# Optimization experiments

Measured on AMD Instinct MI355X. Metric: run time of the kernel, lower is better.

Reference implementation:

```python
import jax, jax.numpy as jnp
import numpy as np

T, B, I, H = 128, 256, 512, 1024  # time, batch, input_size, hidden_size


def setup_inputs() -> dict:
    key = jax.random.key(0)
    k1, k2, k3, k4, k5 = jax.random.split(key, 5)
    s = 1.0 / np.sqrt(H)  # matches torch GRUCell uniform(-1/sqrt(H), 1/sqrt(H)) scale
    return {
        "input_seq": jax.random.normal(k1, (T, B, I), dtype=jnp.float32),
        "W_ih": jax.random.uniform(k2, (3 * H, I), minval=-s, maxval=s, dtype=jnp.float32),
        "W_hh": jax.random.uniform(k3, (3 * H, H), minval=-s, maxval=s, dtype=jnp.float32),
        "b_ih": jax.random.uniform(k4, (3 * H,), minval=-s, maxval=s, dtype=jnp.float32),
        "b_hh": jax.random.uniform(k5, (3 * H,), minval=-s, maxval=s, dtype=jnp.float32),
    }


def reference(input_seq, W_ih, W_hh, b_ih, b_hh):
    # Original torch code calls GRUCell(input_seq[i]) with NO hidden state and never
    # feeds the output back, so hx = 0 at EVERY step -> no recurrence; fully vectorizable.
    Hd = W_hh.shape[1]
    # input gates for all timesteps at once: (T, B, 3H)
    gi = jnp.einsum('tbi,gi->tbg', input_seq, W_ih) + b_ih
    # hidden gates with hx = 0: zeros @ W_hh.T + b_hh == b_hh broadcast, shape (B, 3H)
    h0 = jnp.zeros((input_seq.shape[1], Hd), dtype=input_seq.dtype)
    gh = h0 @ W_hh.T + b_hh
    i_r, i_z, i_n = gi[..., :Hd], gi[..., Hd:2 * Hd], gi[..., 2 * Hd:]
    h_r, h_z, h_n = gh[..., :Hd], gh[..., Hd:2 * Hd], gh[..., 2 * Hd:]
    r = jax.nn.sigmoid(i_r + h_r)
    z = jax.nn.sigmoid(i_z + h_z)
    n = jnp.tanh(i_n + r * h_n)
    h = (1.0 - z) * n + z * h0  # z*h0 == 0, kept for faithfulness
    # torch.stack(output, dim=1) -> (B, T, H)
    return jnp.transpose(h, (1, 0, 2))
```

## Files before the change

kernel.cpp:

```cpp
#include <hip/hip_runtime.h>
#include <hip/hip_bf16.h>

using f32x4  = __attribute__((ext_vector_type(4))) float;
using bf16x8 = __attribute__((ext_vector_type(8))) short;
using s16x4  = __attribute__((ext_vector_type(4))) short;

#define TT 128
#define BB 256
#define II 512
#define HH 1024
#define MM (TT * BB)

__device__ __forceinline__ short f2bf(float f) {
    unsigned u = __float_as_uint(f);
    u = u + 0x7FFFu + ((u >> 16) & 1u);
    return (short)(u >> 16);
}

__device__ __forceinline__ float sigmoid_f(float x) {
    float e = __expf(-fabsf(x));
    float s = 1.0f / (1.0f + e);
    return x >= 0.0f ? s : 1.0f - s;
}

__device__ __forceinline__ float tanh_f(float x) {
    float e = __expf(-2.0f * fabsf(x));
    float t = (1.0f - e) / (1.0f + e);
    return x >= 0.0f ? t : -t;
}

__device__ __forceinline__ void gload_lds16(const void* g, void* l) {
    __builtin_amdgcn_global_load_lds((const __attribute__((address_space(1))) unsigned*)g,
                                     (__attribute__((address_space(3))) unsigned*)l,
                                     16, 0, 0);
}

__global__ __launch_bounds__(256)
void cvt_both_kernel(const float* __restrict__ A, const float* __restrict__ W,
                     short* __restrict__ dst, int nA8, int nTot8) {
    const int stride = gridDim.x * blockDim.x;
    for (int i = blockIdx.x * blockDim.x + threadIdx.x; i < nTot8; i += stride) {
        const float* src = (i < nA8) ? (A + (size_t)i * 8) : (W + (size_t)(i - nA8) * 8);
        f32x4 v0 = ((const f32x4*)src)[0];
        f32x4 v1 = ((const f32x4*)src)[1];
        bf16x8 o;
        o[0] = f2bf(v0.x); o[1] = f2bf(v0.y); o[2] = f2bf(v0.z); o[3] = f2bf(v0.w);
        o[4] = f2bf(v1.x); o[5] = f2bf(v1.y); o[6] = f2bf(v1.z); o[7] = f2bf(v1.w);
        ((bf16x8*)dst)[i] = o;
    }
}

__global__ __launch_bounds__(512, 2)
void gru_gemm8_kernel(const short* __restrict__ Abf,
                      const short* __restrict__ Wbf,
                      const float* __restrict__ bih,
                      const float* __restrict__ bhh,
                      float* __restrict__ out)
{
    __shared__ char lds[114688];

    const int tid  = threadIdx.x;
    const int wid  = tid >> 6;
    const int lane = tid & 63;
    const int l15  = lane & 15;
    const int l4   = lane >> 4;
    const int wm   = wid >> 1;
    const int wn   = wid & 1;

    const int mtile = blockIdx.x >> 4;
    const int htile = blockIdx.x & 15;
    const int m0 = mtile * 256;
    const int h0 = htile * 64;

    const int lr8 = lane >> 3;
    const int lc  = lane & 7;
    const int csw = (lc * 16) ^ (lr8 << 4);

    const char* Ab = (const char*)Abf;
    const char* Wb = (const char*)Wbf;

    size_t aAddr[4];
    size_t wAddr[3];
    #pragma unroll
    for (int j = 0; j < 4; ++j)
        aAddr[j] = (size_t)(m0 + (wid * 4 + j) * 8 + lr8) * 1024 + csw;
    #pragma unroll
    for (int j = 0; j < 3; ++j) {
        const int row = (wid * 3 + j) * 8 + lr8;
        const int g   = row >> 6;
        const int wr  = row & 63;
        wAddr[j] = (size_t)(g * HH + h0 + wr) * 1024 + csw;
    }

    f32x4 acc[4][3][2];
    #pragma unroll
    for (int mf = 0; mf < 4; ++mf)
        #pragma unroll
        for (int g = 0; g < 3; ++g)
            #pragma unroll
            for (int nf = 0; nf < 2; ++nf)
                acc[mf][g][nf] = (f32x4){0.f, 0.f, 0.f, 0.f};

    #define STAGE(t, p)                                                          \
        do {                                                                     \
            const int kb_ = (t) * 128;                                           \
            _Pragma("unroll")                                                    \
            for (int j = 0; j < 4; ++j)                                          \
                gload_lds16(Ab + aAddr[j] + kb_,                                 \
                            lds + (p) * 32768 + (wid * 4 + j) * 1024);           \
            _Pragma("unroll")                                                    \
            for (int j = 0; j < 3; ++j)                                          \
                gload_lds16(Wb + wAddr[j] + kb_,                                 \
                            lds + 65536 + (p) * 24576 + (wid * 3 + j) * 1024);   \
        } while (0)

    STAGE(0, 0);

    const int xsw = (l15 & 7) << 4;

    for (int t = 0; t < 8; ++t) {
        const int p = t & 1;
        if (t < 7) {
            STAGE(t + 1, p ^ 1);
            asm volatile("s_waitcnt vmcnt(7)" ::: "memory");
        } else {
            asm volatile("s_waitcnt vmcnt(0)" ::: "memory");
        }
        __builtin_amdgcn_s_barrier();

        const char* Abase = lds + p * 32768;
        const char* Wbase = lds + 65536 + p * 24576;

        #pragma unroll
        for (int kk = 0; kk < 2; ++kk) {
            const int cb = kk * 64 + l4 * 16;
            bf16x8 a[4], b[3][2];
            #pragma unroll
            for (int mf = 0; mf < 4; ++mf) {
                const int r = wm * 64 + mf * 16 + l15;
                a[mf] = *(const bf16x8*)(Abase + r * 128 + (cb ^ xsw));
            }
            #pragma unroll
            for (int g = 0; g < 3; ++g)
                #pragma unroll
                for (int nf = 0; nf < 2; ++nf) {
                    const int rn = g * 64 + wn * 32 + nf * 16 + l15;
                    b[g][nf] = *(const bf16x8*)(Wbase + rn * 128 + (cb ^ xsw));
                }
            __builtin_amdgcn_s_setprio(1);
            #pragma unroll
            for (int mf = 0; mf < 4; ++mf)
                #pragma unroll
                for (int g = 0; g < 3; ++g)
                    #pragma unroll
                    for (int nf = 0; nf < 2; ++nf)
                        acc[mf][g][nf] = __builtin_amdgcn_mfma_f32_16x16x32_bf16(
                            a[mf], b[g][nf], acc[mf][g][nf], 0, 0, 0);
            __builtin_amdgcn_s_setprio(0);
        }
        asm volatile("" ::: "memory");
        __builtin_amdgcn_s_barrier();
    }
    #undef STAGE

    #pragma unroll
    for (int nf = 0; nf < 2; ++nf) {
        const int h = h0 + wn * 32 + nf * 16 + l15;
        const float bir = bih[h]          + bhh[h];
        const float biz = bih[HH + h]     + bhh[HH + h];
        const float bin = bih[2 * HH + h];
        const float bhn = bhh[2 * HH + h];
        #pragma unroll
        for (int mf = 0; mf < 4; ++mf) {
            const f32x4 ra = acc[mf][0][nf];
            const f32x4 za = acc[mf][1][nf];
            const f32x4 na = acc[mf][2][nf];
            #pragma unroll
            for (int j = 0; j < 4; ++j) {
                const int m = m0 + wm * 64 + mf * 16 + l4 * 4 + j;
                const int tt = m >> 8;
                const int bb = m & 255;
                const float r = sigmoid_f(ra[j] + bir);
                const float z = sigmoid_f(za[j] + biz);
                const float n = tanh_f(na[j] + bin + r * bhn);
                out[(size_t)bb * (TT * HH) + (size_t)tt * HH + h] = (1.0f - z) * n;
            }
        }
    }
}

__global__ __launch_bounds__(256, 2)
void gru_fused_kernel(const float* __restrict__ A,
                      const float* __restrict__ Wih,
                      const float* __restrict__ bih,
                      const float* __restrict__ bhh,
                      float* __restrict__ out)
{
    __shared__ short As[128 * 64];
    __shared__ short Ws[192 * 64];

    const int tid  = threadIdx.x;
    const int wid  = tid >> 6;
    const int lane = tid & 63;
    const int l15  = lane & 15;
    const int l4   = lane >> 4;

    const int mtile = blockIdx.x >> 4;
    const int htile = blockIdx.x & 15;
    const int m0 = mtile * 128;
    const int h0 = htile * 64;

    const int rbase = tid >> 4;
    const int c4    = tid & 15;
    const int swz   = (rbase & 7) << 3;

    f32x4 acc[2][12];
    #pragma unroll
    for (int i = 0; i < 2; ++i)
        #pragma unroll
        for (int j = 0; j < 12; ++j)
            acc[i][j] = (f32x4){0.f, 0.f, 0.f, 0.f};

    for (int kt = 0; kt < II / 64; ++kt) {
        const int k0 = kt * 64;
        __syncthreads();
        const float* Ab = A + (size_t)(m0 + rbase) * II + k0 + c4 * 4;
        #pragma unroll
        for (int i = 0; i < 8; ++i) {
            f32x4 v = *(const f32x4*)(Ab + (size_t)i * 16 * II);
            s16x4 hv;
            hv.x = f2bf(v.x); hv.y = f2bf(v.y); hv.z = f2bf(v.z); hv.w = f2bf(v.w);
            *(s16x4*)(As + (i * 16 + rbase) * 64 + ((c4 * 4) ^ swz)) = hv;
        }
        #pragma unroll
        for (int i = 0; i < 12; ++i) {
            const int row = i * 16 + rbase;
            const int g   = row >> 6;
            const int r   = row & 63;
            f32x4 v = *(const f32x4*)(Wih + (size_t)(g * HH + h0 + r) * II + k0 + c4 * 4);
            s16x4 hv;
            hv.x = f2bf(v.x); hv.y = f2bf(v.y); hv.z = f2bf(v.z); hv.w = f2bf(v.w);
            *(s16x4*)(Ws + row * 64 + ((c4 * 4) ^ swz)) = hv;
        }
        __syncthreads();

        #pragma unroll
        for (int kk = 0; kk < 2; ++kk) {
            const int kc = kk * 32 + l4 * 8;
            const int r0 = wid * 32 + l15;
            bf16x8 a0 = *(const bf16x8*)(As + r0 * 64 + (kc ^ ((r0 & 7) << 3)));
            bf16x8 a1 = *(const bf16x8*)(As + (r0 + 16) * 64 + (kc ^ ((r0 & 7) << 3)));
            #pragma unroll
            for (int nf = 0; nf < 12; ++nf) {
                const int rn = nf * 16 + l15;
                bf16x8 b = *(const bf16x8*)(Ws + rn * 64 + (kc ^ ((rn & 7) << 3)));
                acc[0][nf] = __builtin_amdgcn_mfma_f32_16x16x32_bf16(a0, b, acc[0][nf], 0, 0, 0);
                acc[1][nf] = __builtin_amdgcn_mfma_f32_16x16x32_bf16(a1, b, acc[1][nf], 0, 0, 0);
            }
        }
    }

    #pragma unroll
    for (int nf = 0; nf < 4; ++nf) {
        const int h = h0 + nf * 16 + l15;
        const float bir = bih[h]          + bhh[h];
        const float biz = bih[HH + h]     + bhh[HH + h];
        const float bin = bih[2 * HH + h];
        const float bhn = bhh[2 * HH + h];
        #pragma unroll
        for (int mf = 0; mf < 2; ++mf) {
            const f32x4 ra = acc[mf][nf];
            const f32x4 za = acc[mf][nf + 4];
            const f32x4 na = acc[mf][nf + 8];
            #pragma unroll
            for (int j = 0; j < 4; ++j) {
                const int m = m0 + wid * 32 + mf * 16 + l4 * 4 + j;
                const int tt = m >> 8;
                const int bb = m & 255;
                const float r = sigmoid_f(ra[j] + bir);
                const float z = sigmoid_f(za[j] + biz);
                const float n = tanh_f(na[j] + bin + r * bhn);
                out[(size_t)bb * (TT * HH) + (size_t)tt * HH + h] = (1.0f - z) * n;
            }
        }
    }
}

extern "C" void kernel_launch(void* const* d_in, const int* in_sizes, int n_in,
                              void* d_out, int out_size, void* d_ws, size_t ws_size,
                              hipStream_t stream) {
    const float* input = (const float*)d_in[0];
    const float* Wih   = (const float*)d_in[1];
    const float* bih   = (const float*)d_in[3];
    const float* bhh   = (const float*)d_in[4];
    float* out = (float*)d_out;

    const size_t nA = (size_t)MM * II;
    const size_t nW = (size_t)3 * HH * II;
    const size_t need = (nA + nW) * sizeof(short);

    if (ws_size >= need) {
        short* Abf = (short*)d_ws;
        cvt_both_kernel<<<4096, 256, 0, stream>>>(input, Wih, Abf,
                                                  (int)(nA / 8), (int)((nA + nW) / 8));
        const int nblocks = (MM / 256) * (HH / 64);
        gru_gemm8_kernel<<<nblocks, 512, 0, stream>>>(Abf, Abf + nA, bih, bhh, out);
    } else {
        const int nblocks = (MM / 128) * (HH / 64);
        gru_fused_kernel<<<nblocks, 256, 0, stream>>>(input, Wih, bih, bhh, out);
    }
}
```

Before: 341.2 us.

## Interleave global-to-LDS loads with MFMA phases and triple-buffer weights

Splits each K-tile of the GEMM into four MFMA phases and issues the next tile's A loads and the tile-after-next's W loads between them, with a triple-buffered W region in LDS (LDS grows to 136 KB). This is meant to hide global load latency behind matrix math rather than staging a whole tile up front. It also flips the block-index mapping so consecutive blocks share the same weight tile and walk different M tiles, which changes L2 reuse. The cost is more barriers per tile, and the larger LDS footprint may limit how many blocks fit on each CU.

```diff
diff --git a/kernel.cpp b/kernel.cpp
--- a/kernel.cpp
+++ b/kernel.cpp
@@ -51,13 +51,13 @@
 }
 
 __global__ __launch_bounds__(512, 2)
-void gru_gemm8_kernel(const short* __restrict__ Abf,
-                      const short* __restrict__ Wbf,
-                      const float* __restrict__ bih,
-                      const float* __restrict__ bhh,
-                      float* __restrict__ out)
+void gru_gemm8p_kernel(const short* __restrict__ Abf,
+                       const short* __restrict__ Wbf,
+                       const float* __restrict__ bih,
+                       const float* __restrict__ bhh,
+                       float* __restrict__ out)
 {
-    __shared__ char lds[114688];
+    __shared__ char lds[139264];
 
     const int tid  = threadIdx.x;
     const int wid  = tid >> 6;
@@ -67,8 +67,8 @@
     const int wm   = wid >> 1;
     const int wn   = wid & 1;
 
-    const int mtile = blockIdx.x >> 4;
-    const int htile = blockIdx.x & 15;
+    const int mtile = blockIdx.x & 127;
+    const int htile = blockIdx.x >> 7;
     const int m0 = mtile * 256;
     const int h0 = htile * 64;
 
@@ -92,6 +92,13 @@
         wAddr[j] = (size_t)(g * HH + h0 + wr) * 1024 + csw;
     }
 
+#define ABUF(p) ((char*)lds + (p) * 32768)
+#define WBUF(q) ((char*)lds + 65536 + (q) * 24576)
+#define GLA(u1, j) gload_lds16(Ab + aAddr[j] + (size_t)(u1) * 128, \
+                               ABUF((u1) & 1) + (wid * 4 + (j)) * 1024)
+#define GLW(u2, j) gload_lds16(Wb + wAddr[j] + (size_t)(u2) * 128, \
+                               WBUF((u2) % 3) + (wid * 3 + (j)) * 1024)
+
     f32x4 acc[4][3][2];
     #pragma unroll
     for (int mf = 0; mf < 4; ++mf)
@@ -101,67 +108,78 @@
             for (int nf = 0; nf < 2; ++nf)
                 acc[mf][g][nf] = (f32x4){0.f, 0.f, 0.f, 0.f};
 
-    #define STAGE(t, p)                                                          \
-        do {                                                                     \
-            const int kb_ = (t) * 128;                                           \
-            _Pragma("unroll")                                                    \
-            for (int j = 0; j < 4; ++j)                                          \
-                gload_lds16(Ab + aAddr[j] + kb_,                                 \
-                            lds + (p) * 32768 + (wid * 4 + j) * 1024);           \
-            _Pragma("unroll")                                                    \
-            for (int j = 0; j < 3; ++j)                                          \
-                gload_lds16(Wb + wAddr[j] + kb_,                                 \
-                            lds + 65536 + (p) * 24576 + (wid * 3 + j) * 1024);   \
-        } while (0)
-
-    STAGE(0, 0);
+    #pragma unroll
+    for (int j = 0; j < 3; ++j) GLW(0, j);
+    #pragma unroll
+    for (int j = 0; j < 4; ++j) GLA(0, j);
+    #pragma unroll
+    for (int j = 0; j < 3; ++j) GLW(1, j);
+    asm volatile("s_waitcnt vmcnt(3)" ::: "memory");
+    __builtin_amdgcn_s_barrier();
 
     const int xsw = (l15 & 7) << 4;
 
-    for (int t = 0; t < 8; ++t) {
-        const int p = t & 1;
-        if (t < 7) {
-            STAGE(t + 1, p ^ 1);
-            asm volatile("s_waitcnt vmcnt(7)" ::: "memory");
-        } else {
-            asm volatile("s_waitcnt vmcnt(0)" ::: "memory");
-        }
+#define PHASE_TAIL(NH)                                                        \
+    __builtin_amdgcn_s_barrier();                                             \
+    asm volatile("s_waitcnt lgkmcnt(0)" ::: "memory");                        \
+    __builtin_amdgcn_sched_barrier(0);                                        \
+    __builtin_amdgcn_s_setprio(1);                                            \
+    _Pragma("unroll")                                                         \
+    for (int mf = 0; mf < 4; ++mf)                                            \
+        _Pragma("unroll")                                                     \
+        for (int g = 0; g < 3; ++g)                                           \
+            acc[mf][g][NH] = __builtin_amdgcn_mfma_f32_16x16x32_bf16(         \
+                a[mf], b[g], acc[mf][g][NH], 0, 0, 0);                        \
+    __builtin_amdgcn_s_setprio(0);
+
+    #pragma unroll
+    for (int u = 0; u < 8; ++u) {
+        const char* Al = ABUF(u & 1);
+        const char* Wl = WBUF(u % 3);
+        bf16x8 a[4], b[3];
+
+        #pragma unroll
+        for (int mf = 0; mf < 4; ++mf)
+            a[mf] = *(const bf16x8*)(Al + (wm * 64 + mf * 16 + l15) * 128 + ((l4 * 16) ^ xsw));
+        #pragma unroll
+        for (int g = 0; g < 3; ++g)
+            b[g] = *(const bf16x8*)(Wl + (g * 64 + wn * 32 + l15) * 128 + ((l4 * 16) ^ xsw));
+        if (u < 7) { GLA(u + 1, 0); GLA(u + 1, 1); }
+        PHASE_TAIL(0)
         __builtin_amdgcn_s_barrier();
 
-        const char* Abase = lds + p * 32768;
-        const char* Wbase = lds + 65536 + p * 24576;
-
-        #pragma unroll
-        for (int kk = 0; kk < 2; ++kk) {
-            const int cb = kk * 64 + l4 * 16;
-            bf16x8 a[4], b[3][2];
-            #pragma unroll
-            for (int mf = 0; mf < 4; ++mf) {
-                const int r = wm * 64 + mf * 16 + l15;
-                a[mf] = *(const bf16x8*)(Abase + r * 128 + (cb ^ xsw));
-            }
-            #pragma unroll
-            for (int g = 0; g < 3; ++g)
-                #pragma unroll
-                for (int nf = 0; nf < 2; ++nf) {
-                    const int rn = g * 64 + wn * 32 + nf * 16 + l15;
-                    b[g][nf] = *(const bf16x8*)(Wbase + rn * 128 + (cb ^ xsw));
-                }
-            __builtin_amdgcn_s_setprio(1);
-            #pragma unroll
-            for (int mf = 0; mf < 4; ++mf)
-                #pragma unroll
-                for (int g = 0; g < 3; ++g)
-                    #pragma unroll
-                    for (int nf = 0; nf < 2; ++nf)
-                        acc[mf][g][nf] = __builtin_amdgcn_mfma_f32_16x16x32_bf16(
-                            a[mf], b[g][nf], acc[mf][g][nf], 0, 0, 0);
-            __builtin_amdgcn_s_setprio(0);
-        }
-        asm volatile("" ::: "memory");
+        #pragma unroll
+        for (int g = 0; g < 3; ++g)
+            b[g] = *(const bf16x8*)(Wl + (g * 64 + wn * 32 + 16 + l15) * 128 + ((l4 * 16) ^ xsw));
+        if (u < 7) { GLA(u + 1, 2); GLA(u + 1, 3); }
+        if (u < 6) { GLW(u + 2, 0); }
+        PHASE_TAIL(1)
         __builtin_amdgcn_s_barrier();
-    }
-    #undef STAGE
+
+        #pragma unroll
+        for (int mf = 0; mf < 4; ++mf)
+            a[mf] = *(const bf16x8*)(Al + (wm * 64 + mf * 16 + l15) * 128 + ((64 + l4 * 16) ^ xsw));
+        #pragma unroll
+        for (int g = 0; g < 3; ++g)
+            b[g] = *(const bf16x8*)(Wl + (g * 64 + wn * 32 + l15) * 128 + ((64 + l4 * 16) ^ xsw));
+        if (u < 6) { GLW(u + 2, 1); }
+        PHASE_TAIL(0)
+        __builtin_amdgcn_s_barrier();
+
+        #pragma unroll
+        for (int g = 0; g < 3; ++g)
+            b[g] = *(const bf16x8*)(Wl + (g * 64 + wn * 32 + 16 + l15) * 128 + ((64 + l4 * 16) ^ xsw));
+        if (u < 6) { GLW(u + 2, 2); }
+        PHASE_TAIL(1)
+        if (u < 6)      asm volatile("s_waitcnt vmcnt(3)" ::: "memory");
+        else if (u == 6) asm volatile("s_waitcnt vmcnt(0)" ::: "memory");
+        __builtin_amdgcn_s_barrier();
+    }
+#undef PHASE_TAIL
+#undef GLA
+#undef GLW
+#undef ABUF
+#undef WBUF
 
     #pragma unroll
     for (int nf = 0; nf < 2; ++nf) {
@@ -224,10 +242,10 @@
     for (int kt = 0; kt < II / 64; ++kt) {
         const int k0 = kt * 64;
         __syncthreads();
-        const float* Ab = A + (size_t)(m0 + rbase) * II + k0 + c4 * 4;
+        const float* Abp = A + (size_t)(m0 + rbase) * II + k0 + c4 * 4;
         #pragma unroll
         for (int i = 0; i < 8; ++i) {
-            f32x4 v = *(const f32x4*)(Ab + (size_t)i * 16 * II);
+            f32x4 v = *(const f32x4*)(Abp + (size_t)i * 16 * II);
             s16x4 hv;
             hv.x = f2bf(v.x); hv.y = f2bf(v.y); hv.z = f2bf(v.z); hv.w = f2bf(v.w);
             *(s16x4*)(As + (i * 16 + rbase) * 64 + ((c4 * 4) ^ swz)) = hv;
@@ -304,7 +322,7 @@
         cvt_both_kernel<<<4096, 256, 0, stream>>>(input, Wih, Abf,
                                                   (int)(nA / 8), (int)((nA + nW) / 8));
         const int nblocks = (MM / 256) * (HH / 64);
-        gru_gemm8_kernel<<<nblocks, 512, 0, stream>>>(Abf, Abf + nA, bih, bhh, out);
+        gru_gemm8p_kernel<<<nblocks, 512, 0, stream>>>(Abf, Abf + nA, bih, bhh, out);
     } else {
         const int nblocks = (MM / 128) * (HH / 64);
         gru_fused_kernel<<<nblocks, 256, 0, stream>>>(input, Wih, bih, bhh, out);
```

Measured after the change: 344.5 us. About the same (+1.0%).

## Shrink GEMM block tile to 128x192 with 4 waves and interleaved LDS loads

Applied to the files above, without the earlier changes.

Replaces the 8-wave 256-row block with a 4-wave, 128-row block in which each wave covers 32 rows against all 192 gate columns. LDS drops from 112 KB to 80 KB, and the grid becomes M-fastest so that blocks sharing a weight tile run together. The inner loop now interleaves each B-fragment LDS read with two MFMAs, and sched_barrier fences are added. The goal is better occupancy and latency hiding, at the cost of less A-tile reuse per block, since W is now loaded twice as often in total.

```diff
diff --git a/kernel.cpp b/kernel.cpp
--- a/kernel.cpp
+++ b/kernel.cpp
@@ -50,26 +50,24 @@
     }
 }
 
-__global__ __launch_bounds__(512, 2)
-void gru_gemm8_kernel(const short* __restrict__ Abf,
-                      const short* __restrict__ Wbf,
-                      const float* __restrict__ bih,
-                      const float* __restrict__ bhh,
-                      float* __restrict__ out)
+__global__ __launch_bounds__(256, 2)
+void gru_gemm_db_kernel(const short* __restrict__ Abf,
+                        const short* __restrict__ Wbf,
+                        const float* __restrict__ bih,
+                        const float* __restrict__ bhh,
+                        float* __restrict__ out)
 {
-    __shared__ char lds[114688];
+    __shared__ char lds[81920];
 
     const int tid  = threadIdx.x;
     const int wid  = tid >> 6;
     const int lane = tid & 63;
     const int l15  = lane & 15;
     const int l4   = lane >> 4;
-    const int wm   = wid >> 1;
-    const int wn   = wid & 1;
-
-    const int mtile = blockIdx.x >> 4;
-    const int htile = blockIdx.x & 15;
-    const int m0 = mtile * 256;
+
+    const int mtile = blockIdx.x & 255;
+    const int htile = blockIdx.x >> 8;
+    const int m0 = mtile * 128;
     const int h0 = htile * 64;
 
     const int lr8 = lane >> 3;
@@ -80,104 +78,91 @@
     const char* Wb = (const char*)Wbf;
 
     size_t aAddr[4];
-    size_t wAddr[3];
+    size_t wAddr[6];
     #pragma unroll
     for (int j = 0; j < 4; ++j)
         aAddr[j] = (size_t)(m0 + (wid * 4 + j) * 8 + lr8) * 1024 + csw;
     #pragma unroll
-    for (int j = 0; j < 3; ++j) {
-        const int row = (wid * 3 + j) * 8 + lr8;
+    for (int j = 0; j < 6; ++j) {
+        const int row = (wid * 6 + j) * 8 + lr8;
         const int g   = row >> 6;
         const int wr  = row & 63;
         wAddr[j] = (size_t)(g * HH + h0 + wr) * 1024 + csw;
     }
 
-    f32x4 acc[4][3][2];
-    #pragma unroll
-    for (int mf = 0; mf < 4; ++mf)
-        #pragma unroll
-        for (int g = 0; g < 3; ++g)
-            #pragma unroll
-            for (int nf = 0; nf < 2; ++nf)
-                acc[mf][g][nf] = (f32x4){0.f, 0.f, 0.f, 0.f};
-
-    #define STAGE(t, p)                                                          \
-        do {                                                                     \
-            const int kb_ = (t) * 128;                                           \
-            _Pragma("unroll")                                                    \
-            for (int j = 0; j < 4; ++j)                                          \
-                gload_lds16(Ab + aAddr[j] + kb_,                                 \
-                            lds + (p) * 32768 + (wid * 4 + j) * 1024);           \
-            _Pragma("unroll")                                                    \
-            for (int j = 0; j < 3; ++j)                                          \
-                gload_lds16(Wb + wAddr[j] + kb_,                                 \
-                            lds + 65536 + (p) * 24576 + (wid * 3 + j) * 1024);   \
-        } while (0)
+#define STAGE(t, p)                                                           \
+    do {                                                                      \
+        const int kb_ = (t) * 128;                                            \
+        _Pragma("unroll")                                                     \
+        for (int j = 0; j < 4; ++j)                                           \
+            gload_lds16(Ab + aAddr[j] + kb_,                                  \
+                        lds + (p) * 16384 + (wid * 4 + j) * 1024);            \
+        _Pragma("unroll")                                                     \
+        for (int j = 0; j < 6; ++j)                                           \
+            gload_lds16(Wb + wAddr[j] + kb_,                                  \
+                        lds + 32768 + (p) * 24576 + (wid * 6 + j) * 1024);    \
+    } while (0)
+
+    f32x4 acc[2][12];
+    #pragma unroll
+    for (int i = 0; i < 2; ++i)
+        #pragma unroll
+        for (int j = 0; j < 12; ++j)
+            acc[i][j] = (f32x4){0.f, 0.f, 0.f, 0.f};
 
     STAGE(0, 0);
 
     const int xsw = (l15 & 7) << 4;
 
+    #pragma unroll
     for (int t = 0; t < 8; ++t) {
         const int p = t & 1;
         if (t < 7) {
             STAGE(t + 1, p ^ 1);
-            asm volatile("s_waitcnt vmcnt(7)" ::: "memory");
+            asm volatile("s_waitcnt vmcnt(10)" ::: "memory");
         } else {
             asm volatile("s_waitcnt vmcnt(0)" ::: "memory");
         }
         __builtin_amdgcn_s_barrier();
-
-        const char* Abase = lds + p * 32768;
-        const char* Wbase = lds + 65536 + p * 24576;
+        __builtin_amdgcn_sched_barrier(0);
+
+        const char* Al = lds + p * 16384;
+        const char* Wl = lds + 32768 + p * 24576;
 
         #pragma unroll
         for (int kk = 0; kk < 2; ++kk) {
             const int cb = kk * 64 + l4 * 16;
-            bf16x8 a[4], b[3][2];
-            #pragma unroll
-            for (int mf = 0; mf < 4; ++mf) {
-                const int r = wm * 64 + mf * 16 + l15;
-                a[mf] = *(const bf16x8*)(Abase + r * 128 + (cb ^ xsw));
-            }
-            #pragma unroll
-            for (int g = 0; g < 3; ++g)
-                #pragma unroll
-                for (int nf = 0; nf < 2; ++nf) {
-                    const int rn = g * 64 + wn * 32 + nf * 16 + l15;
-                    b[g][nf] = *(const bf16x8*)(Wbase + rn * 128 + (cb ^ xsw));
-                }
-            __builtin_amdgcn_s_setprio(1);
-            #pragma unroll
-            for (int mf = 0; mf < 4; ++mf)
-                #pragma unroll
-                for (int g = 0; g < 3; ++g)
-                    #pragma unroll
-                    for (int nf = 0; nf < 2; ++nf)
-                        acc[mf][g][nf] = __builtin_amdgcn_mfma_f32_16x16x32_bf16(
-                            a[mf], b[g][nf], acc[mf][g][nf], 0, 0, 0);
-            __builtin_amdgcn_s_setprio(0);
-        }
-        asm volatile("" ::: "memory");
+            const int r0 = wid * 32 + l15;
+            bf16x8 a0 = *(const bf16x8*)(Al + r0 * 128 + (cb ^ xsw));
+            bf16x8 a1 = *(const bf16x8*)(Al + (r0 + 16) * 128 + (cb ^ xsw));
+            #pragma unroll
+            for (int nf = 0; nf < 12; ++nf) {
+                const int rn = nf * 16 + l15;
+                bf16x8 b = *(const bf16x8*)(Wl + rn * 128 + (cb ^ xsw));
+                acc[0][nf] = __builtin_amdgcn_mfma_f32_16x16x32_bf16(a0, b, acc[0][nf], 0, 0, 0);
+                acc[1][nf] = __builtin_amdgcn_mfma_f32_16x16x32_bf16(a1, b, acc[1][nf], 0, 0, 0);
+            }
+        }
+        __builtin_amdgcn_sched_barrier(0);
         __builtin_amdgcn_s_barrier();
     }
-    #undef STAGE
-
-    #pragma unroll
-    for (int nf = 0; nf < 2; ++nf) {
-        const int h = h0 + wn * 32 + nf * 16 + l15;
+#undef STAGE
+
+    #pragma unroll
+    for (int nf = 0; nf < 4; ++nf) {
+        const int h = h0 + nf * 16 + l15;
         const float bir = bih[h]          + bhh[h];
         const float biz = bih[HH + h]     + bhh[HH + h];
         const float bin = bih[2 * HH + h];
         const float bhn = bhh[2 * HH + h];
         #pragma unroll
-        for (int mf = 0; mf < 4; ++mf) {
-            const f32x4 ra = acc[mf][0][nf];
-            const f32x4 za = acc[mf][1][nf];
-            const f32x4 na = acc[mf][2][nf];
+        for (int mf = 0; mf < 2; ++mf) {
+            const f32x4 ra = acc[mf][nf];
+            const f32x4 za = acc[mf][nf + 4];
+            const f32x4 na = acc[mf][nf + 8];
             #pragma unroll
             for (int j = 0; j < 4; ++j) {
-                const int m = m0 + wm * 64 + mf * 16 + l4 * 4 + j;
+                const int m = m0 + wid * 32 + mf * 16 + l4 * 4 + j;
                 const int tt = m >> 8;
                 const int bb = m & 255;
                 const float r = sigmoid_f(ra[j] + bir);
@@ -224,10 +209,10 @@
     for (int kt = 0; kt < II / 64; ++kt) {
         const int k0 = kt * 64;
         __syncthreads();
-        const float* Ab = A + (size_t)(m0 + rbase) * II + k0 + c4 * 4;
+        const float* Abp = A + (size_t)(m0 + rbase) * II + k0 + c4 * 4;
         #pragma unroll
         for (int i = 0; i < 8; ++i) {
-            f32x4 v = *(const f32x4*)(Ab + (size_t)i * 16 * II);
+            f32x4 v = *(const f32x4*)(Abp + (size_t)i * 16 * II);
             s16x4 hv;
             hv.x = f2bf(v.x); hv.y = f2bf(v.y); hv.z = f2bf(v.z); hv.w = f2bf(v.w);
             *(s16x4*)(As + (i * 16 + rbase) * 64 + ((c4 * 4) ^ swz)) = hv;
@@ -303,8 +288,8 @@
         short* Abf = (short*)d_ws;
         cvt_both_kernel<<<4096, 256, 0, stream>>>(input, Wih, Abf,
                                                   (int)(nA / 8), (int)((nA + nW) / 8));
-        const int nblocks = (MM / 256) * (HH / 64);
-        gru_gemm8_kernel<<<nblocks, 512, 0, stream>>>(Abf, Abf + nA, bih, bhh, out);
+        const int nblocks = (MM / 128) * (HH / 64);
+        gru_gemm_db_kernel<<<nblocks, 256, 0, stream>>>(Abf, Abf + nA, bih, bhh, out);
     } else {
         const int nblocks = (MM / 128) * (HH / 64);
         gru_fused_kernel<<<nblocks, 256, 0, stream>>>(input, Wih, bih, bhh, out);
```

Result: no change. 338.5 us (-0.8%).
